# Performance work log

Hardware: AMD Instinct MI355X
Metric: run time of the kernel (lower is better)

The kernel has to match this reference:

```python
import jax, jax.numpy as jnp
import numpy as np

PATCH_LENGTH = 128
PATCH_STRIDE = 64
WINDOW_SIZE = 16
L = 500000


def setup_inputs() -> dict:
    key = jax.random.key(0)
    k1, k2, k3 = jax.random.split(key, 3)
    I = jax.random.normal(k1, (L,), dtype=jnp.float32)
    Q = jax.random.normal(k2, (L,), dtype=jnp.float32)
    edge_weights = jax.random.normal(k3, (PATCH_LENGTH, PATCH_LENGTH), dtype=jnp.float32)
    return {"I": I, "Q": Q, "edge_weights": edge_weights}


def reference(I, Q, edge_weights):
    pl, stride, ws = PATCH_LENGTH, PATCH_STRIDE, WINDOW_SIZE
    n = I.shape[0]
    P = (n - pl) // stride + 1
    # Gather all patches at once: idx[p, t] = p*stride + t  -> [P, pl]
    idx = jnp.arange(P)[:, None] * stride + jnp.arange(pl)[None, :]
    patches = jnp.stack([I[idx], Q[idx]], axis=-1)  # [P, pl, 2]
    # Banded adjacency computed ONCE (it is identical for every patch):
    # adj[i, j] = sigmoid(edge_weights[i, j]) if 0 < |i - j| <= ws else 0
    r = jnp.arange(pl)
    d = jnp.abs(r[:, None] - r[None, :])
    band_mask = ((d <= ws) & (d > 0)).astype(edge_weights.dtype)  # [pl, pl]
    adj = jax.nn.sigmoid(edge_weights) * band_mask
    adjs = jnp.broadcast_to(adj, (P, pl, pl))  # [P, pl, pl]
    return patches, adjs
```

## Files before the change

### kernel.cpp

```cpp
#include <hip/hip_runtime.h>

#define PATCH_LENGTH 128
#define PATCH_STRIDE 64
#define WINDOW_SIZE 16

__global__ void adj_compute_kernel(const float* __restrict__ ew, float* __restrict__ adj) {
    int idx = blockIdx.x * blockDim.x + threadIdx.x;
    if (idx < PATCH_LENGTH * PATCH_LENGTH) {
        int i = idx >> 7;
        int j = idx & 127;
        int d = i - j; if (d < 0) d = -d;
        float s = 1.0f / (1.0f + expf(-ew[idx]));
        adj[idx] = (d > 0 && d <= WINDOW_SIZE) ? s : 0.0f;
    }
}

__global__ void patches_kernel(const float* __restrict__ I, const float* __restrict__ Q,
                               float2* __restrict__ out, int total) {
    int idx = blockIdx.x * blockDim.x + threadIdx.x;
    if (idx < total) {
        int p = idx >> 7;
        int t = idx & 127;
        int src = p * PATCH_STRIDE + t;
        out[idx] = make_float2(I[src], Q[src]);
    }
}

__global__ void adjs_broadcast_kernel(const float4* __restrict__ adj4, float4* __restrict__ out) {
    const int per_patch4 = PATCH_LENGTH * PATCH_LENGTH / 4;
    float4* dst = out + (size_t)blockIdx.x * per_patch4;
#pragma unroll
    for (int k = 0; k < per_patch4 / 256; ++k) {
        int idx = k * 256 + threadIdx.x;
        dst[idx] = adj4[idx];
    }
}

__global__ void adjs_broadcast_lds_kernel(const float* __restrict__ ew, float4* __restrict__ out) {
    __shared__ float adj[PATCH_LENGTH * PATCH_LENGTH];
    for (int k = threadIdx.x; k < PATCH_LENGTH * PATCH_LENGTH; k += blockDim.x) {
        int i = k >> 7, j = k & 127;
        int d = i - j; if (d < 0) d = -d;
        float s = 1.0f / (1.0f + expf(-ew[k]));
        adj[k] = (d > 0 && d <= WINDOW_SIZE) ? s : 0.0f;
    }
    __syncthreads();
    const int per_patch4 = PATCH_LENGTH * PATCH_LENGTH / 4;
    float4* dst = out + (size_t)blockIdx.x * per_patch4;
    const float4* a4 = reinterpret_cast<const float4*>(adj);
#pragma unroll
    for (int k = 0; k < per_patch4 / 256; ++k) {
        int idx = k * 256 + threadIdx.x;
        dst[idx] = a4[idx];
    }
}

extern "C" void kernel_launch(void* const* d_in, const int* in_sizes, int n_in,
                              void* d_out, int out_size, void* d_ws, size_t ws_size,
                              hipStream_t stream) {
    const float* I  = (const float*)d_in[0];
    const float* Q  = (const float*)d_in[1];
    const float* ew = (const float*)d_in[2];
    float* out = (float*)d_out;

    const int n = in_sizes[0];
    const int P = (n - PATCH_LENGTH) / PATCH_STRIDE + 1;

    const int totalPT = P * PATCH_LENGTH;
    patches_kernel<<<(totalPT + 255) / 256, 256, 0, stream>>>(I, Q, (float2*)out, totalPT);

    float* adj_out = out + (size_t)P * PATCH_LENGTH * 2;

    if (ws_size >= (size_t)PATCH_LENGTH * PATCH_LENGTH * sizeof(float)) {
        float* adj = (float*)d_ws;
        adj_compute_kernel<<<(PATCH_LENGTH * PATCH_LENGTH + 255) / 256, 256, 0, stream>>>(ew, adj);
        adjs_broadcast_kernel<<<P, 256, 0, stream>>>((const float4*)adj, (float4*)adj_out);
    } else {
        adjs_broadcast_lds_kernel<<<P, 256, 0, stream>>>(ew, (float4*)adj_out);
    }
}
```

Before: 106.9 us.

## Fuse patch gather, adjacency compute and broadcast into one register-resident kernel

Replaces three kernels with a single kernel launched over roughly P/4 blocks. Each block first gathers patches with float4 stores, then computes its slice of the banded sigmoid adjacency into registers once and writes it to several patches. This removes the workspace round-trip, repeated adjacency reads and extra launches. Risks are fewer blocks for saturating write bandwidth and higher register pressure from holding 16 float4 values.

```diff
diff --git a/kernel.cpp b/kernel.cpp
--- a/kernel.cpp
+++ b/kernel.cpp
@@ -1,57 +1,53 @@
 #include <hip/hip_runtime.h>
 
-#define PATCH_LENGTH 128
-#define PATCH_STRIDE 64
-#define WINDOW_SIZE 16
+#define PL 128
+#define STRIDE 64
+#define WSZ 16
 
-__global__ void adj_compute_kernel(const float* __restrict__ ew, float* __restrict__ adj) {
-    int idx = blockIdx.x * blockDim.x + threadIdx.x;
-    if (idx < PATCH_LENGTH * PATCH_LENGTH) {
-        int i = idx >> 7;
-        int j = idx & 127;
-        int d = i - j; if (d < 0) d = -d;
-        float s = 1.0f / (1.0f + expf(-ew[idx]));
-        adj[idx] = (d > 0 && d <= WINDOW_SIZE) ? s : 0.0f;
+__global__ __launch_bounds__(256) void fused_kernel(
+    const float* __restrict__ I, const float* __restrict__ Q,
+    const float* __restrict__ ew, float* __restrict__ out, int P)
+{
+    const int tid  = threadIdx.x;
+    const int bid  = blockIdx.x;
+    const int nblk = gridDim.x;
+
+    {
+        float4* pout = reinterpret_cast<float4*>(out);
+        const int total = P * (PL / 2);
+        for (int idx = bid * 256 + tid; idx < total; idx += nblk * 256) {
+            int p = idx >> 6;
+            int t = (idx & 63) * 2;
+            int src = p * STRIDE + t;
+            pout[idx] = make_float4(I[src], Q[src], I[src + 1], Q[src + 1]);
+        }
     }
-}
 
-__global__ void patches_kernel(const float* __restrict__ I, const float* __restrict__ Q,
-                               float2* __restrict__ out, int total) {
-    int idx = blockIdx.x * blockDim.x + threadIdx.x;
-    if (idx < total) {
-        int p = idx >> 7;
-        int t = idx & 127;
-        int src = p * PATCH_STRIDE + t;
-        out[idx] = make_float2(I[src], Q[src]);
+    float4 v[16];
+#pragma unroll
+    for (int k = 0; k < 16; ++k) {
+        const int i  = k * 8 + (tid >> 5);
+        const int j0 = (tid & 31) * 4;
+        float4 r = make_float4(0.f, 0.f, 0.f, 0.f);
+        float* rp = &r.x;
+#pragma unroll
+        for (int c = 0; c < 4; ++c) {
+            int j = j0 + c;
+            int d = i - j; if (d < 0) d = -d;
+            if (d > 0 && d <= WSZ) {
+                rp[c] = 1.0f / (1.0f + __expf(-ew[i * PL + j]));
+            }
+        }
+        v[k] = r;
     }
-}
 
-__global__ void adjs_broadcast_kernel(const float4* __restrict__ adj4, float4* __restrict__ out) {
-    const int per_patch4 = PATCH_LENGTH * PATCH_LENGTH / 4;
-    float4* dst = out + (size_t)blockIdx.x * per_patch4;
+    float4* aout = reinterpret_cast<float4*>(out + (size_t)P * PL * 2);
+    for (int p = bid; p < P; p += nblk) {
+        float4* dst = aout + (size_t)p * (PL * PL / 4);
 #pragma unroll
-    for (int k = 0; k < per_patch4 / 256; ++k) {
-        int idx = k * 256 + threadIdx.x;
-        dst[idx] = adj4[idx];
-    }
-}
-
-__global__ void adjs_broadcast_lds_kernel(const float* __restrict__ ew, float4* __restrict__ out) {
-    __shared__ float adj[PATCH_LENGTH * PATCH_LENGTH];
-    for (int k = threadIdx.x; k < PATCH_LENGTH * PATCH_LENGTH; k += blockDim.x) {
-        int i = k >> 7, j = k & 127;
-        int d = i - j; if (d < 0) d = -d;
-        float s = 1.0f / (1.0f + expf(-ew[k]));
-        adj[k] = (d > 0 && d <= WINDOW_SIZE) ? s : 0.0f;
-    }
-    __syncthreads();
-    const int per_patch4 = PATCH_LENGTH * PATCH_LENGTH / 4;
-    float4* dst = out + (size_t)blockIdx.x * per_patch4;
-    const float4* a4 = reinterpret_cast<const float4*>(adj);
-#pragma unroll
-    for (int k = 0; k < per_patch4 / 256; ++k) {
-        int idx = k * 256 + threadIdx.x;
-        dst[idx] = a4[idx];
+        for (int k = 0; k < 16; ++k) {
+            dst[k * 256 + tid] = v[k];
+        }
     }
 }
 
@@ -64,18 +60,8 @@
     float* out = (float*)d_out;
 
     const int n = in_sizes[0];
-    const int P = (n - PATCH_LENGTH) / PATCH_STRIDE + 1;
+    const int P = (n - PL) / STRIDE + 1;
 
-    const int totalPT = P * PATCH_LENGTH;
-    patches_kernel<<<(totalPT + 255) / 256, 256, 0, stream>>>(I, Q, (float2*)out, totalPT);
-
-    float* adj_out = out + (size_t)P * PATCH_LENGTH * 2;
-
-    if (ws_size >= (size_t)PATCH_LENGTH * PATCH_LENGTH * sizeof(float)) {
-        float* adj = (float*)d_ws;
-        adj_compute_kernel<<<(PATCH_LENGTH * PATCH_LENGTH + 255) / 256, 256, 0, stream>>>(ew, adj);
-        adjs_broadcast_kernel<<<P, 256, 0, stream>>>((const float4*)adj, (float4*)adj_out);
-    } else {
-        adjs_broadcast_lds_kernel<<<P, 256, 0, stream>>>(ew, (float4*)adj_out);
-    }
+    const int nblk = (P + 3) / 4;
+    fused_kernel<<<nblk, 256, 0, stream>>>(I, Q, ew, out, P);
 }
```

After: 112.8 us. +5.5%, slower.
